# Optimization experiments

Hardware: AMD Instinct MI355X
Metric: run time of the kernel (lower is better)

## Reference

```python
import jax, jax.numpy as jnp
import numpy as np

B, S, D = 2, 2048, 4096
H, KVH, HD = 32, 8, 128
N_REP = H // KVH
ROPE_THETA = 10000.0


def setup_inputs() -> dict:
    key = jax.random.key(0)
    ks = jax.random.split(key, 6)
    x_norm = jax.random.normal(ks[0], (B, S, D), dtype=jnp.float32)
    scale = 0.02
    wq = jax.random.normal(ks[1], (H * HD, D), dtype=jnp.float32) * scale
    wk = jax.random.normal(ks[2], (KVH * HD, D), dtype=jnp.float32) * scale
    wv = jax.random.normal(ks[3], (KVH * HD, D), dtype=jnp.float32) * scale
    wo = jax.random.normal(ks[4], (D, H * HD), dtype=jnp.float32) * scale
    # RoPE tables: freqs_cis[t, j] = exp(i * t * theta^{-2j/HD})
    inv_freq = 1.0 / (ROPE_THETA ** (jnp.arange(0, HD, 2, dtype=jnp.float32) / HD))  # [HD/2]
    angles = jnp.arange(S, dtype=jnp.float32)[:, None] * inv_freq[None, :]  # [S, HD/2]
    freqs_cos = jnp.cos(angles)
    freqs_sin = jnp.sin(angles)
    # causal additive mask (0 on/below diagonal, -1e9 above)
    mask = jnp.where(jnp.arange(S)[None, :] > jnp.arange(S)[:, None], jnp.float32(-1e9), jnp.float32(0.0))
    return {"x_norm": x_norm, "wq": wq, "wk": wk, "wv": wv, "wo": wo,
            "freqs_cos": freqs_cos, "freqs_sin": freqs_sin, "mask": mask, "start_pos": 0}


def _apply_rope(t, cos, sin):
    # t: [B, S, h, HD]; cos/sin: [S, HD/2] -> rotate consecutive pairs
    tr = t.reshape(*t.shape[:-1], HD // 2, 2)
    t0, t1 = tr[..., 0], tr[..., 1]
    c = cos[None, :, None, :]
    s = sin[None, :, None, :]
    out = jnp.stack([t0 * c - t1 * s, t0 * s + t1 * c], axis=-1)
    return out.reshape(t.shape)


def reference(x_norm, wq, wk, wv, wo, freqs_cos, freqs_sin, mask, start_pos):
    # QKV projections (torch Linear: y = x @ W.T)
    xq = jnp.einsum("bsd,ed->bse", x_norm, wq).reshape(B, S, H, HD)
    xk = jnp.einsum("bsd,ed->bse", x_norm, wk).reshape(B, S, KVH, HD)
    xv = jnp.einsum("bsd,ed->bse", x_norm, wv).reshape(B, S, KVH, HD)
    xq = _apply_rope(xq, freqs_cos, freqs_sin)
    xk = _apply_rope(xk, freqs_cos, freqs_sin)
    # start_pos == 0 prefill: cache slice [:start_pos+seqlen] == freshly written xk/xv
    keys = jnp.repeat(xk, N_REP, axis=2)    # [B, S, H, HD] (GQA repeat_kv)
    values = jnp.repeat(xv, N_REP, axis=2)  # [B, S, H, HD]
    scale = 1.0 / np.sqrt(HD).astype(np.float32)
    scores = jnp.einsum("bqhd,bkhd->bhqk", xq, keys) * scale
    scores = scores + mask[None, None, :, :]
    probs = jax.nn.softmax(scores.astype(jnp.float32), axis=-1).astype(xq.dtype)
    out = jnp.einsum("bhqk,bkhd->bqhd", probs, values).reshape(B, S, H * HD)
    return jnp.einsum("bse,de->bsd", out, wo)
```

## Files before the change

### kernel.cpp

```cpp
#include <hip/hip_runtime.h>
#include <stdint.h>

#define B_N 2
#define S_N 2048
#define D_N 4096
#define H_N 32
#define KVH_N 8
#define HD_N 128
#define NQT (S_N / 64)
#define QS_LOG2E 0.12751743f

typedef __attribute__((ext_vector_type(8))) short bf16x8;
typedef __attribute__((ext_vector_type(4))) float f32x4;

__device__ __forceinline__ unsigned short f2bf(float f) {
    union { float f; unsigned u; } v; v.f = f;
    unsigned u = v.u;
    u += 0x7fffu + ((u >> 16) & 1u);
    return (unsigned short)(u >> 16);
}
__device__ __forceinline__ float bf2f(unsigned short h) {
    union { unsigned u; float f; } v; v.u = ((unsigned)h) << 16;
    return v.f;
}
__device__ __forceinline__ unsigned cvt_pk_bf16(float lo, float hi) {
    unsigned r;
    asm("v_cvt_pk_bf16_f32 %0, %1, %2" : "=v"(r) : "v"(lo), "v"(hi));
    return r;
}

__device__ __forceinline__ void gl16(const unsigned short* g, unsigned short* l) {
    __builtin_amdgcn_global_load_lds(
        (const __attribute__((address_space(1))) void*)g,
        (__attribute__((address_space(3))) void*)l, 16, 0, 0);
}

__global__ void __launch_bounds__(256) conv_f32_bf16(const float* __restrict__ in,
                                                     unsigned short* __restrict__ out) {
    int i = (blockIdx.x * 256 + threadIdx.x) * 4;
    float4 v = *(const float4*)(in + i);
    ushort4 o;
    o.x = f2bf(v.x); o.y = f2bf(v.y); o.z = f2bf(v.z); o.w = f2bf(v.w);
    *(ushort4*)(out + i) = o;
}

#define BAR() __builtin_amdgcn_s_barrier()
#define VMC4() asm volatile("s_waitcnt vmcnt(4)" ::: "memory")
#define VMC2() asm volatile("s_waitcnt vmcnt(2)" ::: "memory")

template<int MODE>
__global__ void __launch_bounds__(512, 2)
gemm256(const unsigned short* __restrict__ A, const unsigned short* __restrict__ Bm,
        void* __restrict__ Cv, int M, int N, int K,
        const float* __restrict__ fc, const float* __restrict__ fs) {
    __shared__ unsigned short ldsA[2][16384];
    __shared__ unsigned short ldsB[2][16384];

    const int tid = threadIdx.x;
    const int lane = tid & 63;
    const int w = tid >> 6;
    const int li = lane & 15, lg = lane >> 4;
    const int wr = w >> 2, wc = w & 3;

    const int nwg = gridDim.x;
    const int cpx = nwg >> 3;
    const int wg = (blockIdx.x & 7) * cpx + (blockIdx.x >> 3);
    const int nbn = N >> 8;
    const int bm = wg / nbn, bn = wg - bm * nbn;
    const int m0 = bm << 8, n0 = bn << 8;

    const int rbase = ((tid >> 7) << 4) + ((tid >> 2) & 15);
    const int cstg = ((tid >> 6) & 1) * 32 + (((tid & 3) * 8) ^ (((tid >> 5) & 1) << 4));
    const unsigned short* Abase = A + (size_t)(m0 + rbase) * K + cstg;
    const unsigned short* Bbase = Bm + (size_t)(n0 + rbase) * K + cstg;
    const int dstoff = tid * 8;
    const int kmask = K - 1;

    f32x4 acc[8][4];
#pragma unroll
    for (int i = 0; i < 8; ++i)
#pragma unroll
        for (int j = 0; j < 4; ++j) acc[i][j] = (f32x4){0.f, 0.f, 0.f, 0.f};

    const int colpart = (lg * 16) ^ ((li >> 3) << 5);

#define STG(BASE, LDSBUF, H, T) do {                                              \
        int kk_ = ((T) * 64) & kmask;                                             \
        gl16(BASE + (size_t)(((H) * 2 + 0) * 64) * K + kk_,                       \
             &LDSBUF[((H) * 2 + 0) * 4096 + dstoff]);                             \
        gl16(BASE + (size_t)(((H) * 2 + 1) * 64) * K + kk_,                       \
             &LDSBUF[((H) * 2 + 1) * 4096 + dstoff]);                             \
    } while (0)

#define LDBs(set, buf) do {                                                       \
        _Pragma("unroll")                                                         \
        for (int ni_ = 0; ni_ < 4; ++ni_) {                                       \
            _Pragma("unroll")                                                     \
            for (int ks_ = 0; ks_ < 2; ++ks_)                                     \
                bfr[set][ni_][ks_] = *(const bf16x8*)((const char*)&ldsB[buf][0]  \
                    + (wc * 4 + ni_) * 2048 + ks_ * 1024 + li * 64 + colpart);    \
        }                                                                         \
    } while (0)

#define LDAs(set, buf, q) do {                                                    \
        _Pragma("unroll")                                                         \
        for (int m_ = 0; m_ < 2; ++m_) {                                          \
            _Pragma("unroll")                                                     \
            for (int ks_ = 0; ks_ < 2; ++ks_)                                     \
                af[set][m_][ks_] = *(const bf16x8*)((const char*)&ldsA[buf][0]    \
                    + (wr * 8 + (q) * 2 + m_) * 2048 + ks_ * 1024 + li * 64 + colpart); \
        }                                                                         \
    } while (0)

#define MFMAs(sb, sa, q) do {                                                     \
        __builtin_amdgcn_s_setprio(1);                                            \
        _Pragma("unroll")                                                         \
        for (int ks_ = 0; ks_ < 2; ++ks_) {                                       \
            _Pragma("unroll")                                                     \
            for (int m_ = 0; m_ < 2; ++m_) {                                      \
                _Pragma("unroll")                                                 \
                for (int ni_ = 0; ni_ < 4; ++ni_)                                 \
                    acc[(q) * 2 + m_][ni_] = __builtin_amdgcn_mfma_f32_16x16x32_bf16( \
                        af[sa][m_][ks_], bfr[sb][ni_][ks_], acc[(q) * 2 + m_][ni_], 0, 0, 0); \
            }                                                                     \
        }                                                                         \
        __builtin_amdgcn_s_setprio(0);                                            \
    } while (0)

    STG(Abase, ldsA[0], 0, 0); STG(Abase, ldsA[0], 1, 0);
    STG(Bbase, ldsB[0], 0, 0); STG(Bbase, ldsB[0], 1, 0);
    STG(Bbase, ldsB[1], 0, 1); STG(Bbase, ldsB[1], 1, 1);
    VMC4();
    BAR();

    bf16x8 bfr[2][4][2], af[2][2][2];
    LDBs(0, 0);
    LDAs(0, 0, 0);

    const int NIT = K >> 7;
#pragma unroll 1
    for (int i = 0; i < NIT; ++i) {
        const int T = 2 * i;
        LDAs(1, 0, 1);
        STG(Abase, ldsA[1], 0, T + 1);
        MFMAs(0, 0, 0);
        BAR();
        LDAs(0, 0, 2);
        STG(Abase, ldsA[1], 1, T + 1);
        STG(Bbase, ldsB[0], 0, T + 2);
        MFMAs(0, 1, 1);
        BAR();
        LDAs(1, 0, 3);
        STG(Bbase, ldsB[0], 1, T + 2);
        MFMAs(0, 0, 2);
        VMC4();
        BAR();
        LDBs(1, 1);
        LDAs(0, 1, 0);
        MFMAs(0, 1, 3);
        BAR();
        LDAs(1, 1, 1);
        STG(Abase, ldsA[0], 0, T + 2);
        MFMAs(1, 0, 0);
        BAR();
        LDAs(0, 1, 2);
        STG(Abase, ldsA[0], 1, T + 2);
        STG(Bbase, ldsB[1], 0, T + 3);
        MFMAs(1, 1, 1);
        BAR();
        LDAs(1, 1, 3);
        STG(Bbase, ldsB[1], 1, T + 3);
        MFMAs(1, 0, 2);
        VMC4();
        BAR();
        LDBs(0, 0);
        LDAs(0, 0, 0);
        MFMAs(1, 1, 3);
        BAR();
    }

    const int r0 = m0 + wr * 128 + lg * 4;
    const int c0 = n0 + wc * 64 + li;
    if (MODE == 1) {
        float* C = (float*)Cv;
#pragma unroll
        for (int mi = 0; mi < 8; ++mi)
#pragma unroll
            for (int ni = 0; ni < 4; ++ni)
#pragma unroll
                for (int rr = 0; rr < 4; ++rr)
                    C[(size_t)(r0 + mi * 16 + rr) * N + c0 + ni * 16] = acc[mi][ni][rr];
    } else if (MODE == 0) {
        unsigned short* C = (unsigned short*)Cv;
#pragma unroll
        for (int mi = 0; mi < 8; ++mi)
#pragma unroll
            for (int ni = 0; ni < 4; ++ni)
#pragma unroll
                for (int rr = 0; rr < 4; ++rr)
                    C[(size_t)(r0 + mi * 16 + rr) * N + c0 + ni * 16] = f2bf(acc[mi][ni][rr]);
    } else {
        unsigned short* C = (unsigned short*)Cv;
        const float sgn = (li & 1) ? 1.f : -1.f;
#pragma unroll
        for (int mi = 0; mi < 8; ++mi)
#pragma unroll
            for (int rr = 0; rr < 4; ++rr) {
                const int row = r0 + mi * 16 + rr;
                const int sidx = (row & (S_N - 1)) * 64;
#pragma unroll
                for (int ni = 0; ni < 4; ++ni) {
                    const int col = c0 + ni * 16;
                    const int ii = sidx + ((col & 127) >> 1);
                    float v = acc[mi][ni][rr];
                    float p = __shfl_xor(v, 1);
                    float o = (v * fc[ii] + sgn * p * fs[ii]) * QS_LOG2E;
                    C[(size_t)row * N + col] = f2bf(o);
                }
            }
    }
#undef STG
#undef LDBs
#undef LDAs
#undef MFMAs
}

template<int ROPEK>
__global__ void __launch_bounds__(512, 2)
gemm256x128(const unsigned short* __restrict__ A, const unsigned short* __restrict__ Bm,
            void* __restrict__ Cv, int M, int N, int K,
            const float* __restrict__ fc, const float* __restrict__ fs) {
    __shared__ unsigned short ldsA[2][16384];
    __shared__ unsigned short ldsB[2][8192];

    const int tid = threadIdx.x;
    const int lane = tid & 63;
    const int w = tid >> 6;
    const int li = lane & 15, lg = lane >> 4;
    const int wr = w >> 1, wc = w & 1;

    const int nwg = gridDim.x;
    const int cpx = nwg >> 3;
    const int wg = (blockIdx.x & 7) * cpx + (blockIdx.x >> 3);
    const int nbn = N >> 7;
    const int bm = wg / nbn, bn = wg - bm * nbn;
    const int m0 = bm << 8, n0 = bn << 7;

    const int rbase = ((tid >> 7) << 4) + ((tid >> 2) & 15);
    const int cstg = ((tid >> 6) & 1) * 32 + (((tid & 3) * 8) ^ (((tid >> 5) & 1) << 4));
    const unsigned short* Asrc[4];
    const unsigned short* Bsrc[2];
#pragma unroll
    for (int hj = 0; hj < 4; ++hj)
        Asrc[hj] = A + (size_t)(m0 + hj * 64 + rbase) * K + cstg;
#pragma unroll
    for (int hj = 0; hj < 2; ++hj)
        Bsrc[hj] = Bm + (size_t)(n0 + hj * 64 + rbase) * K + cstg;
    const int dstoff = tid * 8;
    const int kmask = K - 1;

    f32x4 acc[4][4];
#pragma unroll
    for (int i = 0; i < 4; ++i)
#pragma unroll
        for (int j = 0; j < 4; ++j) acc[i][j] = (f32x4){0.f, 0.f, 0.f, 0.f};

    const int colpart = (lg * 16) ^ ((li >> 3) << 5);

#define STG2(SRC, LDSBUF, H, T) do {                                        \
        int kk_ = ((T) * 64) & kmask;                                       \
        gl16(SRC[(H)*2 + 0] + kk_, &LDSBUF[((H)*2 + 0) * 4096 + dstoff]);   \
        gl16(SRC[(H)*2 + 1] + kk_, &LDSBUF[((H)*2 + 1) * 4096 + dstoff]);   \
    } while (0)

#define LDB2(buf) do {                                                       \
        _Pragma("unroll")                                                    \
        for (int ni_ = 0; ni_ < 4; ++ni_) {                                  \
            _Pragma("unroll")                                                \
            for (int ks_ = 0; ks_ < 2; ++ks_)                                \
                bfr[ni_][ks_] = *(const bf16x8*)((const char*)&ldsB[buf][0]  \
                    + (wc * 4 + ni_) * 2048 + ks_ * 1024 + li * 64 + colpart); \
        }                                                                    \
    } while (0)

#define LDA2(buf, q) do {                                                    \
        _Pragma("unroll")                                                    \
        for (int ks_ = 0; ks_ < 2; ++ks_)                                    \
            af2[ks_] = *(const bf16x8*)((const char*)&ldsA[buf][0]           \
                + (wr * 4 + (q)) * 2048 + ks_ * 1024 + li * 64 + colpart);   \
    } while (0)

#define MFMA8(q) do {                                                        \
        __builtin_amdgcn_s_setprio(1);                                       \
        _Pragma("unroll")                                                    \
        for (int ks_ = 0; ks_ < 2; ++ks_) {                                  \
            _Pragma("unroll")                                                \
            for (int ni_ = 0; ni_ < 4; ++ni_)                                \
                acc[q][ni_] = __builtin_amdgcn_mfma_f32_16x16x32_bf16(       \
                    af2[ks_], bfr[ni_][ks_], acc[q][ni_], 0, 0, 0);          \
        }                                                                    \
        __builtin_amdgcn_s_setprio(0);                                       \
    } while (0)

    STG2(Asrc, ldsA[0], 0, 0); STG2(Asrc, ldsA[0], 1, 0);
    STG2(Bsrc, ldsB[0], 0, 0);
    STG2(Bsrc, ldsB[1], 0, 1);
    VMC2();
    BAR();

    const int NIT = K >> 7;
    bf16x8 bfr[4][2], af2[2];
#pragma unroll 1
    for (int i = 0; i < NIT; ++i) {
        const int T = 2 * i;
        LDB2(0); LDA2(0, 0);
        STG2(Asrc, ldsA[1], 0, T + 1);
        BAR(); MFMA8(0); BAR();
        LDA2(0, 1);
        STG2(Asrc, ldsA[1], 1, T + 1);
        BAR(); MFMA8(1); BAR();
        LDA2(0, 2);
        STG2(Bsrc, ldsB[0], 0, T + 2);
        BAR(); MFMA8(2); BAR();
        LDA2(0, 3);
        VMC2();
        BAR(); MFMA8(3); BAR();
        LDB2(1); LDA2(1, 0);
        STG2(Asrc, ldsA[0], 0, T + 2);
        BAR(); MFMA8(0); BAR();
        LDA2(1, 1);
        STG2(Asrc, ldsA[0], 1, T + 2);
        BAR(); MFMA8(1); BAR();
        LDA2(1, 2);
        STG2(Bsrc, ldsB[1], 0, T + 3);
        BAR(); MFMA8(2); BAR();
        LDA2(1, 3);
        VMC2();
        BAR(); MFMA8(3); BAR();
    }

    const int r0 = m0 + wr * 64 + lg * 4;
    const int c0 = n0 + wc * 64 + li;
    unsigned short* C = (unsigned short*)Cv;
    if (ROPEK && bn < 8) {
        const float sgn = (li & 1) ? 1.f : -1.f;
#pragma unroll
        for (int mi = 0; mi < 4; ++mi)
#pragma unroll
            for (int rr = 0; rr < 4; ++rr) {
                const int row = r0 + mi * 16 + rr;
                const int sidx = (row & (S_N - 1)) * 64;
#pragma unroll
                for (int ni = 0; ni < 4; ++ni) {
                    const int col = c0 + ni * 16;
                    const int ii = sidx + ((col & 127) >> 1);
                    float v = acc[mi][ni][rr];
                    float p = __shfl_xor(v, 1);
                    float o = v * fc[ii] + sgn * p * fs[ii];
                    C[(size_t)row * N + col] = f2bf(o);
                }
            }
    } else {
#pragma unroll
        for (int mi = 0; mi < 4; ++mi)
#pragma unroll
            for (int ni = 0; ni < 4; ++ni)
#pragma unroll
                for (int rr = 0; rr < 4; ++rr)
                    C[(size_t)(r0 + mi * 16 + rr) * N + c0 + ni * 16] = f2bf(acc[mi][ni][rr]);
    }
#undef STG2
#undef LDB2
#undef LDA2
#undef MFMA8
}

__device__ __forceinline__ void stage_k8(const unsigned short* kt_base,
                                         unsigned short* ks_base, int w, int lane) {
#pragma unroll
    for (int j = 0; j < 2; ++j) {
        int row = (w * 2 + j) * 4 + (lane >> 4);
        int colb = (lane & 15) * 16;
        int key = (row & 7) << 4;
        gl16(kt_base + (size_t)row * 2048 + ((colb ^ key) >> 1),
             ks_base + (w * 2 + j) * 512);
    }
}

__device__ __forceinline__ void load_v(const unsigned short* vt_base, int tid, uint4& a0, uint4& a1) {
    int kv = (tid >> 4) * 2, d0 = (tid & 15) * 8;
    const unsigned short* vp = vt_base + (size_t)kv * 2048 + d0;
    a0 = *(const uint4*)vp;
    a1 = *(const uint4*)(vp + 2048);
}

__device__ __forceinline__ void write_v(unsigned short* vt_lds, int tid, uint4 a0, uint4 a1) {
    int kv = (tid >> 4) * 2, d0 = (tid & 15) * 8;
    union { uint4 q; unsigned short u[8]; } x0, x1;
    x0.q = a0; x1.q = a1;
#pragma unroll
    for (int jj = 0; jj < 8; ++jj) {
        int d = d0 + jj;
        unsigned pack = (unsigned)x0.u[jj] | ((unsigned)x1.u[jj] << 16);
        int key = ((d ^ (d >> 3)) & 7) << 4;
        *(unsigned*)((char*)vt_lds + d * 128 + ((kv * 2) ^ key)) = pack;
    }
}

__global__ void __launch_bounds__(512, 2) attn_kernel(const unsigned short* __restrict__ Q,
                                                      const unsigned short* __restrict__ Kb,
                                                      const unsigned short* __restrict__ Vb,
                                                      unsigned short* __restrict__ O) {
    __shared__ unsigned short Ks[2][64 * 128];
    __shared__ unsigned short Vt[2][128 * 64];

    const int pidx = blockIdx.x;
    const int bg = blockIdx.y;
    const int b = bg >> 3, kvh = bg & 7;
    const int tid = threadIdx.x;
    const int w = tid >> 6, lane = tid & 63;
    const int li = lane & 15, lg = lane >> 4;
    const int h = kvh * 4 + (w >> 1);
    const int qh = (w & 1) * 32;

    const unsigned short* KVrow0 = Kb + (size_t)b * S_N * 2048 + kvh * 128;
    const unsigned short* Vrow0  = Vb + (size_t)b * S_N * 2048 + kvh * 128;

#pragma unroll 1
    for (int pass = 0; pass < 2; ++pass) {
        const int qt = pass ? (NQT - 1 - pidx) : pidx;
        const int nt = qt + 1;

        bf16x8 qf[2][4];
        {
            const unsigned short* qp = Q + ((size_t)b * S_N + qt * 64 + qh + li) * (H_N * HD_N)
                                         + h * HD_N + lg * 8;
#pragma unroll
            for (int mi = 0; mi < 2; ++mi)
#pragma unroll
                for (int ds = 0; ds < 4; ++ds)
                    qf[mi][ds] = *(const bf16x8*)(qp + (size_t)mi * 16 * (H_N * HD_N) + ds * 32);
        }

        float mreg[2], lreg[2];
#pragma unroll
        for (int mi = 0; mi < 2; ++mi) { mreg[mi] = -1e30f; lreg[mi] = 0.f; }
        f32x4 o_acc[2][8];
#pragma unroll
        for (int mi = 0; mi < 2; ++mi)
#pragma unroll
            for (int di = 0; di < 8; ++di) o_acc[mi][di] = (f32x4){0.f, 0.f, 0.f, 0.f};

        {
            stage_k8(KVrow0, &Ks[0][0], w, lane);
            uint4 a0, a1;
            load_v(Vrow0, tid, a0, a1);
            write_v(&Vt[0][0], tid, a0, a1);
        }
        __syncthreads();

#pragma unroll 1
        for (int t = 0; t < nt; ++t) {
            const int c = t & 1;
            const bool pre = (t + 1 < nt);
            uint4 a0, a1;
            if (pre) {
                stage_k8(KVrow0 + (size_t)(t + 1) * 64 * 2048, &Ks[c ^ 1][0], w, lane);
                load_v(Vrow0 + (size_t)(t + 1) * 64 * 2048, tid, a0, a1);
            }

            f32x4 sT[2][4];
#pragma unroll
            for (int mi = 0; mi < 2; ++mi)
#pragma unroll
                for (int ni = 0; ni < 4; ++ni) sT[mi][ni] = (f32x4){0.f, 0.f, 0.f, 0.f};
            __builtin_amdgcn_s_setprio(1);
#pragma unroll
            for (int ni = 0; ni < 4; ++ni) {
                const int kvc = ni * 16 + li;
                const int kkey = (kvc & 7) << 4;
                bf16x8 kf[4];
#pragma unroll
                for (int ds = 0; ds < 4; ++ds)
                    kf[ds] = *(const bf16x8*)((char*)&Ks[c][0] + kvc * 256
                                              + ((ds * 64 + lg * 16) ^ kkey));
#pragma unroll
                for (int mi = 0; mi < 2; ++mi)
#pragma unroll
                    for (int ds = 0; ds < 4; ++ds)
                        sT[mi][ni] = __builtin_amdgcn_mfma_f32_16x16x32_bf16(kf[ds], qf[mi][ds], sT[mi][ni], 0, 0, 0);
            }
            __builtin_amdgcn_s_setprio(0);

            if (t == qt) {
#pragma unroll
                for (int mi = 0; mi < 2; ++mi) {
                    int qq = qh + mi * 16 + li;
#pragma unroll
                    for (int ni = 0; ni < 4; ++ni)
#pragma unroll
                        for (int r = 0; r < 4; ++r)
                            if (ni * 16 + lg * 4 + r > qq) sT[mi][ni][r] = -1e30f;
                }
            }

            float fac0[2];
#pragma unroll
            for (int mi = 0; mi < 2; ++mi) {
                float pm = sT[mi][0][0];
#pragma unroll
                for (int ni = 0; ni < 4; ++ni)
#pragma unroll
                    for (int r = 0; r < 4; ++r) pm = fmaxf(pm, sT[mi][ni][r]);
                pm = fmaxf(pm, __shfl_xor(pm, 16));
                pm = fmaxf(pm, __shfl_xor(pm, 32));
                float mn = fmaxf(mreg[mi], pm);
                fac0[mi] = __builtin_amdgcn_exp2f(mreg[mi] - mn);
                mreg[mi] = mn;
#pragma unroll
                for (int ni = 0; ni < 4; ++ni)
#pragma unroll
                    for (int r = 0; r < 4; ++r)
                        sT[mi][ni][r] = __builtin_amdgcn_exp2f(sT[mi][ni][r] - mn);
                float rs = 0.f;
#pragma unroll
                for (int ni = 0; ni < 4; ++ni)
#pragma unroll
                    for (int r = 0; r < 4; ++r) rs += sT[mi][ni][r];
                rs += __shfl_xor(rs, 16);
                rs += __shfl_xor(rs, 32);
                lreg[mi] = lreg[mi] * fac0[mi] + rs;
            }

#pragma unroll
            for (int mi = 0; mi < 2; ++mi) {
                float facR[4];
#pragma unroll
                for (int rr = 0; rr < 4; ++rr)
                    facR[rr] = __shfl(fac0[mi], (lg << 4) | (lg * 4 + rr));
#pragma unroll
                for (int di = 0; di < 8; ++di)
#pragma unroll
                    for (int rr = 0; rr < 4; ++rr) o_acc[mi][di][rr] *= facR[rr];
            }

            union U { bf16x8 v; unsigned u[4]; };
            U pa[2][2];
#pragma unroll
            for (int mi = 0; mi < 2; ++mi)
#pragma unroll
                for (int ks = 0; ks < 2; ++ks) {
                    pa[mi][ks].u[0] = cvt_pk_bf16(sT[mi][2 * ks][0], sT[mi][2 * ks][1]);
                    pa[mi][ks].u[1] = cvt_pk_bf16(sT[mi][2 * ks][2], sT[mi][2 * ks][3]);
                    pa[mi][ks].u[2] = cvt_pk_bf16(sT[mi][2 * ks + 1][0], sT[mi][2 * ks + 1][1]);
                    pa[mi][ks].u[3] = cvt_pk_bf16(sT[mi][2 * ks + 1][2], sT[mi][2 * ks + 1][3]);
                }

            __builtin_amdgcn_s_setprio(1);
#pragma unroll
            for (int di = 0; di < 8; ++di) {
                int d = di * 16 + li;
                int vkey = ((d ^ (d >> 3)) & 7) << 4;
                const char* vbase = (const char*)&Vt[c][0] + d * 128;
                bf16x8 vf[2];
#pragma unroll
                for (int ks = 0; ks < 2; ++ks) {
                    union { bf16x8 v; unsigned long long g[2]; } vv;
                    int cb = ks * 64 + lg * 8;
                    vv.g[0] = *(const unsigned long long*)(vbase + (cb ^ vkey));
                    vv.g[1] = *(const unsigned long long*)(vbase + ((cb + 32) ^ vkey));
                    vf[ks] = vv.v;
                }
#pragma unroll
                for (int mi = 0; mi < 2; ++mi)
#pragma unroll
                    for (int ks = 0; ks < 2; ++ks)
                        o_acc[mi][di] = __builtin_amdgcn_mfma_f32_16x16x32_bf16(pa[mi][ks].v, vf[ks], o_acc[mi][di], 0, 0, 0);
            }
            __builtin_amdgcn_s_setprio(0);

            if (pre) write_v(&Vt[c ^ 1][0], tid, a0, a1);
            __syncthreads();
        }

        unsigned short* op = O + ((size_t)b * S_N + qt * 64 + qh + lg * 4) * (H_N * HD_N)
                               + h * HD_N + li;
#pragma unroll
        for (int mi = 0; mi < 2; ++mi) {
            float iv = 1.f / lreg[mi];
            float ivR[4];
#pragma unroll
            for (int rr = 0; rr < 4; ++rr)
                ivR[rr] = __shfl(iv, (lg << 4) | (lg * 4 + rr));
#pragma unroll
            for (int di = 0; di < 8; ++di)
#pragma unroll
                for (int rr = 0; rr < 4; ++rr)
                    op[((size_t)(mi * 16 + rr)) * (H_N * HD_N) + di * 16]
                        = f2bf(o_acc[mi][di][rr] * ivR[rr]);
        }
    }
}

extern "C" void kernel_launch(void* const* d_in, const int* in_sizes, int n_in,
                              void* d_out, int out_size, void* d_ws, size_t ws_size,
                              hipStream_t stream) {
    (void)in_sizes; (void)n_in; (void)out_size; (void)ws_size;
    const float* x  = (const float*)d_in[0];
    const float* wq = (const float*)d_in[1];
    const float* wk = (const float*)d_in[2];
    const float* wv = (const float*)d_in[3];
    const float* wo = (const float*)d_in[4];
    const float* fc = (const float*)d_in[5];
    const float* fs = (const float*)d_in[6];
    float* out = (float*)d_out;

    char* ws = (char*)d_ws;
    unsigned short* xb  = (unsigned short*)(ws);
    unsigned short* wb  = (unsigned short*)(ws + 33554432);
    unsigned short* wkv = (unsigned short*)(ws + 67108864);
    unsigned short* Qb  = (unsigned short*)(ws + 83886080);
    unsigned short* KVb = (unsigned short*)(ws + 117440512);

    const int BS = B_N * S_N;

    conv_f32_bf16<<<dim3(BS * D_N / 1024), 256, 0, stream>>>(x, xb);
    conv_f32_bf16<<<dim3(H_N * HD_N * D_N / 1024), 256, 0, stream>>>(wq, wb);
    conv_f32_bf16<<<dim3(KVH_N * HD_N * D_N / 1024), 256, 0, stream>>>(wk, wkv);
    conv_f32_bf16<<<dim3(KVH_N * HD_N * D_N / 1024), 256, 0, stream>>>(wv, wkv + KVH_N * HD_N * D_N);

    gemm256<2><<<dim3((BS / 256) * (D_N / 256)), 512, 0, stream>>>(xb, wb, Qb, BS, D_N, D_N, fc, fs);
    conv_f32_bf16<<<dim3(D_N * H_N * HD_N / 1024), 256, 0, stream>>>(wo, wb);
    gemm256x128<1><<<dim3((BS / 256) * (2048 / 128)), 512, 0, stream>>>(xb, wkv, KVb, BS, 2048, D_N, fc, fs);

    attn_kernel<<<dim3(NQT / 2, B_N * KVH_N), 512, 0, stream>>>(Qb, KVb, KVb + 1024, Qb);

    gemm256<1><<<dim3((BS / 256) * (D_N / 256)), 512, 0, stream>>>(Qb, wb, out, BS, D_N, D_N, fc, fs);
}
```

Before: 529.2 us.

## Merge input conversions into one launch and add lazy softmax rescaling

Replaces four separate fp32-to-bf16 conversion launches for x, wq, wk and wv with one kernel that picks its source by offset into the contiguous workspace layout. In the attention kernel, the running max is only updated, and the output accumulator only rescaled, when some row's new max exceeds the old one by more than 8 in log2 units. This removes launch overhead and skips most exp/shuffle/multiply rescale work. The cost is a warp-wide vote and branches, plus exp values that can reach up to 2^8 before normalisation, which reduces bf16 P precision headroom.

```diff
diff --git a/kernel.cpp b/kernel.cpp
--- a/kernel.cpp
+++ b/kernel.cpp
@@ -42,6 +42,23 @@
     ushort4 o;
     o.x = f2bf(v.x); o.y = f2bf(v.y); o.z = f2bf(v.z); o.w = f2bf(v.w);
     *(ushort4*)(out + i) = o;
+}
+
+__global__ void __launch_bounds__(256) conv_multi(const float* __restrict__ x,
+                                                  const float* __restrict__ wq,
+                                                  const float* __restrict__ wk,
+                                                  const float* __restrict__ wv,
+                                                  unsigned short* __restrict__ dst) {
+    size_t i = ((size_t)blockIdx.x * 256 + threadIdx.x) * 4;
+    const float* s;
+    if (i < 16777216u)      s = x  + i;
+    else if (i < 33554432u) s = wq + (i - 16777216u);
+    else if (i < 37748736u) s = wk + (i - 33554432u);
+    else                    s = wv + (i - 37748736u);
+    float4 v = *(const float4*)s;
+    ushort4 o;
+    o.x = f2bf(v.x); o.y = f2bf(v.y); o.z = f2bf(v.z); o.w = f2bf(v.w);
+    *(ushort4*)(dst + i) = o;
 }
 
 #define BAR() __builtin_amdgcn_s_barrier()
@@ -505,6 +522,7 @@
             }
 
             float fac0[2];
+            bool resc[2];
 #pragma unroll
             for (int mi = 0; mi < 2; ++mi) {
                 float pm = sT[mi][0][0];
@@ -514,14 +532,18 @@
                     for (int r = 0; r < 4; ++r) pm = fmaxf(pm, sT[mi][ni][r]);
                 pm = fmaxf(pm, __shfl_xor(pm, 16));
                 pm = fmaxf(pm, __shfl_xor(pm, 32));
-                float mn = fmaxf(mreg[mi], pm);
-                fac0[mi] = __builtin_amdgcn_exp2f(mreg[mi] - mn);
-                mreg[mi] = mn;
+                resc[mi] = !__all(pm <= mreg[mi] + 8.0f);
+                fac0[mi] = 1.0f;
+                if (resc[mi]) {
+                    float mn = fmaxf(mreg[mi], pm);
+                    fac0[mi] = __builtin_amdgcn_exp2f(mreg[mi] - mn);
+                    mreg[mi] = mn;
+                }
 #pragma unroll
                 for (int ni = 0; ni < 4; ++ni)
 #pragma unroll
                     for (int r = 0; r < 4; ++r)
-                        sT[mi][ni][r] = __builtin_amdgcn_exp2f(sT[mi][ni][r] - mn);
+                        sT[mi][ni][r] = __builtin_amdgcn_exp2f(sT[mi][ni][r] - mreg[mi]);
                 float rs = 0.f;
 #pragma unroll
                 for (int ni = 0; ni < 4; ++ni)
@@ -534,14 +556,16 @@
 
 #pragma unroll
             for (int mi = 0; mi < 2; ++mi) {
-                float facR[4];
-#pragma unroll
-                for (int rr = 0; rr < 4; ++rr)
-                    facR[rr] = __shfl(fac0[mi], (lg << 4) | (lg * 4 + rr));
-#pragma unroll
-                for (int di = 0; di < 8; ++di)
-#pragma unroll
-                    for (int rr = 0; rr < 4; ++rr) o_acc[mi][di][rr] *= facR[rr];
+                if (resc[mi]) {
+                    float facR[4];
+#pragma unroll
+                    for (int rr = 0; rr < 4; ++rr)
+                        facR[rr] = __shfl(fac0[mi], (lg << 4) | (lg * 4 + rr));
+#pragma unroll
+                    for (int di = 0; di < 8; ++di)
+#pragma unroll
+                        for (int rr = 0; rr < 4; ++rr) o_acc[mi][di][rr] *= facR[rr];
+                }
             }
 
             union U { bf16x8 v; unsigned u[4]; };
@@ -624,10 +648,7 @@
 
     const int BS = B_N * S_N;
 
-    conv_f32_bf16<<<dim3(BS * D_N / 1024), 256, 0, stream>>>(x, xb);
-    conv_f32_bf16<<<dim3(H_N * HD_N * D_N / 1024), 256, 0, stream>>>(wq, wb);
-    conv_f32_bf16<<<dim3(KVH_N * HD_N * D_N / 1024), 256, 0, stream>>>(wk, wkv);
-    conv_f32_bf16<<<dim3(KVH_N * HD_N * D_N / 1024), 256, 0, stream>>>(wv, wkv + KVH_N * HD_N * D_N);
+    conv_multi<<<dim3(41943040u / 1024), 256, 0, stream>>>(x, wq, wk, wv, xb);
 
     gemm256<2><<<dim3((BS / 256) * (D_N / 256)), 512, 0, stream>>>(xb, wb, Qb, BS, D_N, D_N, fc, fs);
     conv_f32_bf16<<<dim3(D_N * H_N * HD_N / 1024), 256, 0, stream>>>(wo, wb);
```

Result: no change. 524.1 us, median of 2 (-1.0%).
